# Optimization experiments

Hardware: AMD Instinct MI355X
Metric: run time of the kernel (lower is better)

The kernel has to match this reference:

```python
import jax, jax.numpy as jnp
import numpy as np

B, S, D, H, DFF = 4, 1024, 1024, 16, 4096
DK = D // H
EPS = 1e-6


def setup_inputs() -> dict:
    key = jax.random.key(0)
    ks = jax.random.split(key, 16)
    sd = 0.02
    inp = {
        "x_v": jax.random.normal(ks[0], (B, S, D), jnp.float32),
        "x_k": jax.random.normal(ks[1], (B, S, D), jnp.float32),
        "x_q": jax.random.normal(ks[2], (B, S, D), jnp.float32),
        "mask": jnp.zeros((B, 1, S), jnp.float32),
        # per-head projections stacked: [H, D, DK]
        "wq": jax.random.normal(ks[3], (H, D, DK), jnp.float32) * sd,
        "bq": jnp.zeros((H, DK), jnp.float32),
        "wk": jax.random.normal(ks[4], (H, D, DK), jnp.float32) * sd,
        "bk": jnp.zeros((H, DK), jnp.float32),
        "wv": jax.random.normal(ks[5], (H, D, DK), jnp.float32) * sd,
        "bv": jnp.zeros((H, DK), jnp.float32),
        "w0": jax.random.normal(ks[6], (D, D), jnp.float32) * sd,
        "b0": jnp.zeros((D,), jnp.float32),
        "ln1_g": jnp.ones((D,), jnp.float32),
        "ln1_b": jnp.zeros((D,), jnp.float32),
        "ff1_w": jax.random.normal(ks[7], (D, DFF), jnp.float32) * sd,
        "ff1_b": jnp.zeros((DFF,), jnp.float32),
        "ff2_w": jax.random.normal(ks[8], (DFF, D), jnp.float32) * sd,
        "ff2_b": jnp.zeros((D,), jnp.float32),
        "ln2_g": jnp.ones((D,), jnp.float32),
        "ln2_b": jnp.zeros((D,), jnp.float32),
    }
    return inp


def layer_norm(x, g, b):
    mu = jnp.mean(x, axis=-1, keepdims=True)
    var = jnp.mean(jnp.square(x - mu), axis=-1, keepdims=True)
    return (x - mu) * jax.lax.rsqrt(var + EPS) * g + b


def reference(x_v, x_k, x_q, mask, wq, bq, wk, bk, wv, bv, w0, b0,
              ln1_g, ln1_b, ff1_w, ff1_b, ff2_w, ff2_b, ln2_g, ln2_b):
    # --- Multi-head attention (heads batched instead of Python loop) ---
    q = jnp.einsum('bsd,hdk->bhsk', x_q, wq) + bq[:, None, :]  # [B,H,S,DK]
    k = jnp.einsum('bsd,hdk->bhsk', x_k, wk) + bk[:, None, :]
    v = jnp.einsum('bsd,hdk->bhsk', x_v, wv) + bv[:, None, :]
    scores = jnp.einsum('bhqk,bhsk->bhqs', q, k) / jnp.sqrt(jnp.float32(DK))
    scores = scores + mask[:, None, :, :] * (-1e9)  # mask broadcast over heads
    attn_w = jax.nn.softmax(scores, axis=-1)        # [B,H,S,S]
    attn = jnp.einsum('bhqs,bhsk->bhqk', attn_w, v)  # [B,H,S,DK]
    concat = attn.transpose(0, 2, 1, 3).reshape(B, S, D)
    mha_out = concat @ w0 + b0
    # --- Residual + LayerNorm 1 (dropout is identity at inference) ---
    sub1 = layer_norm(x_q + mha_out, ln1_g, ln1_b)
    # --- Point-wise FFN ---
    ffn = jax.nn.relu(sub1 @ ff1_w + ff1_b) @ ff2_w + ff2_b
    # --- Residual + LayerNorm 2 ---
    out = layer_norm(sub1 + ffn, ln2_g, ln2_b)
    # original returns the attention weights of the LAST head only
    return out, attn_w[:, -1]
```

## Files before the change

kernel.cpp:

```cpp
#include <hip/hip_runtime.h>
#include <hip/hip_bf16.h>
#include <stdint.h>

#define DEV __device__ __forceinline__

typedef uint16_t u16;
typedef __attribute__((ext_vector_type(8))) short s16x8;
typedef __attribute__((ext_vector_type(8))) unsigned short u16x8;
typedef __attribute__((ext_vector_type(4))) unsigned short u16x4;
typedef __attribute__((ext_vector_type(4))) float f32x4;

constexpr int CB = 4;
constexpr int CS = 1024;
constexpr int CD = 1024;
constexpr int CH = 16;
constexpr int CDFF = 4096;
constexpr int LSTR = 72;

DEV float b2f(u16 u) { union { uint32_t i; float f; } v; v.i = (uint32_t)u << 16; return v.f; }
DEV u16 f2b(float f) {
  union { float f; uint32_t i; } v; v.f = f;
  uint32_t r = v.i + 0x7fffu + ((v.i >> 16) & 1u);
  return (u16)(r >> 16);
}

using as1v = const __attribute__((address_space(1))) void;
using as3v = __attribute__((address_space(3))) void;
DEV void g2l16(const u16* g, u16* l) {
  __builtin_amdgcn_global_load_lds((as1v*)g, (as3v*)l, 16, 0, 0);
}

__global__ void detect_dtype(const uint32_t* __restrict__ w, uint32_t* __restrict__ flag) {
  if (threadIdx.x == 0 && blockIdx.x == 0) {
    flag[0] = (w[0] == 0x3F800000u) ? 1u : 0u;
    flag[1] = 0u;
  }
}

__global__ __launch_bounds__(256)
void cvt3(const void* __restrict__ s0, const void* __restrict__ s1, const void* __restrict__ s2,
          u16* __restrict__ d0, u16* __restrict__ d1, u16* __restrict__ d2,
          const uint32_t* __restrict__ flag)
{
  const void* s = blockIdx.z == 0 ? s0 : (blockIdx.z == 1 ? s1 : s2);
  u16* d        = blockIdx.z == 0 ? d0 : (blockIdx.z == 1 ? d1 : d2);
  size_t i = ((size_t)blockIdx.x * 256 + threadIdx.x) * 4;
  if (flag[0]) {
    const float* f = (const float*)s;
    u16x4 o;
#pragma unroll
    for (int j = 0; j < 4; j++) o[j] = f2b(f[i + j]);
    *(u16x4*)(d + i) = o;
  } else {
    *(u16x4*)(d + i) = *(const u16x4*)((const u16*)s + i);
  }
}

struct SmallCvt {
  const void* src[11];
  u16* dst[11];
  int n[11];
};
__global__ __launch_bounds__(256)
void cvt_small(SmallCvt sc, const uint32_t* __restrict__ flag)
{
  int idx = blockIdx.x * 256 + threadIdx.x;
#pragma unroll
  for (int a = 0; a < 11; a++) {
    if (idx < sc.n[a]) {
      if (flag[0]) sc.dst[a][idx] = f2b(((const float*)sc.src[a])[idx]);
      else         sc.dst[a][idx] = ((const u16*)sc.src[a])[idx];
      return;
    }
    idx -= sc.n[a];
  }
}

__global__ __launch_bounds__(256)
void transpose64d(const void* __restrict__ in, u16* __restrict__ out,
                  int in_rs, long long in_ys, long long in_zs,
                  int out_rs, long long out_ys, long long out_zs,
                  const uint32_t* __restrict__ flag)
{
  int t = blockIdx.x * 256 + threadIdx.x;
  int k  = t & 63;
  int n8 = t >> 6;
  size_t ib = (size_t)blockIdx.z * in_zs + (size_t)blockIdx.y * in_ys
            + (size_t)n8 * 8 * in_rs + k;
  u16* ob = out + (size_t)blockIdx.z * out_zs + (size_t)blockIdx.y * out_ys
                + (size_t)k * out_rs + (size_t)n8 * 8;
  u16x8 v;
  if (flag[0]) {
    const float* f = (const float*)in;
#pragma unroll
    for (int j = 0; j < 8; j++) v[j] = f2b(f[ib + (size_t)j * in_rs]);
  } else {
    const u16* u = (const u16*)in;
#pragma unroll
    for (int j = 0; j < 8; j++) v[j] = u[ib + (size_t)j * in_rs];
  }
  *(u16x8*)ob = v;
}

struct GemmArgs {
  const u16* A[3];
  const u16* Bt[3];
  const u16* bias[3];
  u16* C[3];
  float scales[3];
  int M, N, K;
  int relu;
};

template<int MI, int NI, int WGM, int WGN>
DEV void gemm_body(const GemmArgs& g)
{
  constexpr int BM = WGM * MI * 16;
  constexpr int BN = WGN * NI * 16;
  constexpr int CHA = BM / 32;
  constexpr int CHB = BN / 32;

  const int z = blockIdx.z;
  const u16* __restrict__ A    = g.A[z];
  const u16* __restrict__ Bt   = g.Bt[z];
  const u16* __restrict__ bias = g.bias[z];
  u16* __restrict__ C          = g.C[z];
  const float scale = g.scales[z];
  const int N = g.N, K = g.K;

  __shared__ __align__(16) u16 lA[BM * 64];
  __shared__ __align__(16) u16 lB[BN * 64];

  const int tid  = threadIdx.x;
  const int lane = tid & 63;
  const int wave = tid >> 6;
  const int quad = lane >> 4;
  const int l16  = lane & 15;
  const int sw   = l16 & 7;
  const int wm = (wave / WGN) * MI * 16;
  const int wn = (wave % WGN) * NI * 16;

  const int flat = blockIdx.y * gridDim.x + blockIdx.x;
  const int nY = gridDim.y;
  const size_t bm = (size_t)(flat % nY) * BM;
  const size_t bn = (size_t)(flat / nY) * BN;

  f32x4 acc[MI][NI];
#pragma unroll
  for (int mi = 0; mi < MI; mi++)
#pragma unroll
    for (int ni = 0; ni < NI; ni++)
#pragma unroll
      for (int r = 0; r < 4; r++) acc[mi][ni][r] = 0.f;

  const u16* Ab = A + bm * K;
  const u16* Bb = Bt + bn * K;

  for (int k0 = 0; k0 < K; k0 += 64) {
#pragma unroll
    for (int i = 0; i < CHA; i++) {
      int c = i * 256 + tid;
      int r = c >> 3, j = c & 7;
      g2l16(Ab + (size_t)r * K + k0 + ((j ^ (r & 7)) * 8), lA + c * 8);
    }
#pragma unroll
    for (int i = 0; i < CHB; i++) {
      int c = i * 256 + tid;
      int r = c >> 3, j = c & 7;
      g2l16(Bb + (size_t)r * K + k0 + ((j ^ (r & 7)) * 8), lB + c * 8);
    }
    __syncthreads();
#pragma unroll
    for (int kk = 0; kk < 2; kk++) {
      s16x8 af[MI], bfr[NI];
#pragma unroll
      for (int mi = 0; mi < MI; mi++)
        af[mi] = *(const s16x8*)(lA + (wm + mi * 16 + l16) * 64 + (((kk * 4 + quad) ^ sw) * 8));
#pragma unroll
      for (int ni = 0; ni < NI; ni++)
        bfr[ni] = *(const s16x8*)(lB + (wn + ni * 16 + l16) * 64 + (((kk * 4 + quad) ^ sw) * 8));
#pragma unroll
      for (int mi = 0; mi < MI; mi++)
#pragma unroll
        for (int ni = 0; ni < NI; ni++)
          acc[mi][ni] = __builtin_amdgcn_mfma_f32_16x16x32_bf16(af[mi], bfr[ni], acc[mi][ni], 0, 0, 0);
    }
    __syncthreads();
  }

  float bvals[NI];
#pragma unroll
  for (int ni = 0; ni < NI; ni++) bvals[ni] = b2f(bias[bn + wn + ni * 16 + l16]);
#pragma unroll
  for (int mi = 0; mi < MI; mi++) {
#pragma unroll
    for (int r = 0; r < 4; r++) {
      size_t row = bm + wm + mi * 16 + quad * 4 + r;
      u16* crow = C + row * N + bn + wn;
#pragma unroll
      for (int ni = 0; ni < NI; ni++) {
        float v = (acc[mi][ni][r] + bvals[ni]) * scale;
        if (g.relu) v = fmaxf(v, 0.f);
        crow[ni * 16 + l16] = f2b(v);
      }
    }
  }
}

__global__ __launch_bounds__(256, 4) void gemm_qkv (GemmArgs g) { gemm_body<4, 4, 2, 2>(g); }
__global__ __launch_bounds__(256, 4) void gemm_wo  (GemmArgs g) { gemm_body<2, 2, 2, 2>(g); }
__global__ __launch_bounds__(256, 4) void gemm_ffn1(GemmArgs g) { gemm_body<4, 4, 2, 2>(g); }
__global__ __launch_bounds__(256, 4) void gemm_ffn2(GemmArgs g) { gemm_body<2, 2, 2, 2>(g); }

__global__ __launch_bounds__(256, 4)
void flash_attn(const u16* __restrict__ Qb, const u16* __restrict__ Kb,
                const u16* __restrict__ Vt, const u16* __restrict__ mask,
                u16* __restrict__ O, float* __restrict__ ml)
{
  const int b = blockIdx.z;
  const int h = blockIdx.x & 15;
  const int q0 = (blockIdx.x >> 4) * 64;
  const int tid  = threadIdx.x;
  const int lane = tid & 63, wave = tid >> 6;
  const int quad = lane >> 4, l16 = lane & 15;

  __shared__ __align__(16) u16 lK[64 * LSTR];
  __shared__ __align__(16) u16 lV[64 * LSTR];
  __shared__ __align__(16) u16 lP[4][16 * LSTR];

  s16x8 aq[2];
  {
    const u16* qp = Qb + ((size_t)b * CS + q0 + wave * 16 + l16) * CD + h * 64 + quad * 8;
    aq[0] = *(const s16x8*)qp;
    aq[1] = *(const s16x8*)(qp + 32);
  }

  f32x4 of[4];
  float m_r[4], l_r[4];
#pragma unroll
  for (int nt = 0; nt < 4; nt++)
#pragma unroll
    for (int r = 0; r < 4; r++) of[nt][r] = 0.f;
#pragma unroll
  for (int r = 0; r < 4; r++) { m_r[r] = -3.0e38f; l_r[r] = 0.f; }

  int srow[2], scol[2];
#pragma unroll
  for (int i = 0; i < 2; i++) {
    int c = i * 256 + tid;
    srow[i] = c >> 3;
    scol[i] = (c & 7) * 8;
  }

  const u16* Kbase = Kb + (size_t)b * CS * CD + h * 64;
  const u16* Vbase = Vt + ((size_t)(b * CH + h)) * 64 * CS;
  u16* lPw = lP[wave];

  for (int kt = 0; kt < CS / 64; kt++) {
    u16x8 rk[2], rv[2];
#pragma unroll
    for (int i = 0; i < 2; i++) {
      rk[i] = *(const u16x8*)(Kbase + (size_t)(kt * 64 + srow[i]) * CD + scol[i]);
      rv[i] = *(const u16x8*)(Vbase + (size_t)srow[i] * CS + kt * 64 + scol[i]);
    }
    __syncthreads();
#pragma unroll
    for (int i = 0; i < 2; i++) {
      *(u16x8*)(lK + srow[i] * LSTR + scol[i]) = rk[i];
      *(u16x8*)(lV + srow[i] * LSTR + scol[i]) = rv[i];
    }
    __syncthreads();

    f32x4 sf[4];
#pragma unroll
    for (int ni = 0; ni < 4; ni++)
#pragma unroll
      for (int r = 0; r < 4; r++) sf[ni][r] = 0.f;
#pragma unroll
    for (int kk = 0; kk < 2; kk++) {
#pragma unroll
      for (int ni = 0; ni < 4; ni++) {
        s16x8 bk = *(const s16x8*)(lK + (ni * 16 + l16) * LSTR + kk * 32 + quad * 8);
        sf[ni] = __builtin_amdgcn_mfma_f32_16x16x32_bf16(aq[kk], bk, sf[ni], 0, 0, 0);
      }
    }
#pragma unroll
    for (int ni = 0; ni < 4; ni++) {
      float mv = b2f(mask[(size_t)b * CS + kt * 64 + ni * 16 + l16]) * -1e9f;
#pragma unroll
      for (int r = 0; r < 4; r++) sf[ni][r] += mv;
    }
    float mx[4];
#pragma unroll
    for (int r = 0; r < 4; r++)
      mx[r] = fmaxf(fmaxf(sf[0][r], sf[1][r]), fmaxf(sf[2][r], sf[3][r]));
#pragma unroll
    for (int off = 1; off < 16; off <<= 1)
#pragma unroll
      for (int r = 0; r < 4; r++) mx[r] = fmaxf(mx[r], __shfl_xor(mx[r], off, 16));
    float al[4], ps[4];
#pragma unroll
    for (int r = 0; r < 4; r++) {
      float mn = fmaxf(m_r[r], mx[r]);
      al[r] = __expf(m_r[r] - mn);
      m_r[r] = mn;
      ps[r] = 0.f;
    }
#pragma unroll
    for (int ni = 0; ni < 4; ni++)
#pragma unroll
      for (int r = 0; r < 4; r++) {
        float p = __expf(sf[ni][r] - m_r[r]);
        sf[ni][r] = p;
        ps[r] += p;
      }
#pragma unroll
    for (int off = 1; off < 16; off <<= 1)
#pragma unroll
      for (int r = 0; r < 4; r++) ps[r] += __shfl_xor(ps[r], off, 16);
#pragma unroll
    for (int r = 0; r < 4; r++) l_r[r] = l_r[r] * al[r] + ps[r];
#pragma unroll
    for (int nt = 0; nt < 4; nt++)
#pragma unroll
      for (int r = 0; r < 4; r++) of[nt][r] *= al[r];
#pragma unroll
    for (int ni = 0; ni < 4; ni++)
#pragma unroll
      for (int r = 0; r < 4; r++)
        lPw[(quad * 4 + r) * LSTR + ni * 16 + l16] = f2b(sf[ni][r]);
    __syncthreads();
#pragma unroll
    for (int kk = 0; kk < 2; kk++) {
      s16x8 ap = *(const s16x8*)(lPw + l16 * LSTR + kk * 32 + quad * 8);
#pragma unroll
      for (int nt = 0; nt < 4; nt++) {
        s16x8 bv = *(const s16x8*)(lV + (nt * 16 + l16) * LSTR + kk * 32 + quad * 8);
        of[nt] = __builtin_amdgcn_mfma_f32_16x16x32_bf16(ap, bv, of[nt], 0, 0, 0);
      }
    }
  }

#pragma unroll
  for (int r = 0; r < 4; r++) {
    float inv = 1.f / l_r[r];
    size_t row = q0 + wave * 16 + quad * 4 + r;
    u16* orow = O + ((size_t)b * CS + row) * CD + h * 64;
#pragma unroll
    for (int nt = 0; nt < 4; nt++) orow[nt * 16 + l16] = f2b(of[nt][r] * inv);
    if (h == CH - 1 && l16 == 0) {
      ml[(size_t)b * CS + row] = m_r[r];
      ml[(size_t)CB * CS + (size_t)b * CS + row] = l_r[r];
    }
  }
}

__global__ __launch_bounds__(256)
void attn_probs(const u16* __restrict__ Qb, const u16* __restrict__ Kb,
                const u16* __restrict__ mask, const float* __restrict__ ml,
                void* __restrict__ outbuf, const uint32_t* __restrict__ flag)
{
  const int b = blockIdx.z;
  const int h = CH - 1;
  const int q0 = blockIdx.x * 64;
  const int tid  = threadIdx.x;
  const int lane = tid & 63, wave = tid >> 6;
  const int quad = lane >> 4, l16 = lane & 15;
  const size_t OUT1 = (size_t)CB * CS * CD;
  const bool f32out = flag[0] != 0;

  __shared__ __align__(16) u16 lK[64 * LSTR];

  s16x8 aq[2];
  {
    const u16* qp = Qb + ((size_t)b * CS + q0 + wave * 16 + l16) * CD + h * 64 + quad * 8;
    aq[0] = *(const s16x8*)qp;
    aq[1] = *(const s16x8*)(qp + 32);
  }
  float mr[4], lr[4];
#pragma unroll
  for (int r = 0; r < 4; r++) {
    size_t row = q0 + wave * 16 + quad * 4 + r;
    mr[r] = ml[(size_t)b * CS + row];
    lr[r] = 1.f / ml[(size_t)CB * CS + (size_t)b * CS + row];
  }
  int srow[2], scol[2];
#pragma unroll
  for (int i = 0; i < 2; i++) {
    int c = i * 256 + tid;
    srow[i] = c >> 3;
    scol[i] = (c & 7) * 8;
  }
  const u16* Kbase = Kb + (size_t)b * CS * CD + h * 64;

  for (int kt = 0; kt < CS / 64; kt++) {
    u16x8 rk[2];
#pragma unroll
    for (int i = 0; i < 2; i++)
      rk[i] = *(const u16x8*)(Kbase + (size_t)(kt * 64 + srow[i]) * CD + scol[i]);
    __syncthreads();
#pragma unroll
    for (int i = 0; i < 2; i++)
      *(u16x8*)(lK + srow[i] * LSTR + scol[i]) = rk[i];
    __syncthreads();
    f32x4 sf[4];
#pragma unroll
    for (int ni = 0; ni < 4; ni++)
#pragma unroll
      for (int r = 0; r < 4; r++) sf[ni][r] = 0.f;
#pragma unroll
    for (int kk = 0; kk < 2; kk++) {
#pragma unroll
      for (int ni = 0; ni < 4; ni++) {
        s16x8 bk = *(const s16x8*)(lK + (ni * 16 + l16) * LSTR + kk * 32 + quad * 8);
        sf[ni] = __builtin_amdgcn_mfma_f32_16x16x32_bf16(aq[kk], bk, sf[ni], 0, 0, 0);
      }
    }
#pragma unroll
    for (int ni = 0; ni < 4; ni++) {
      float mv = b2f(mask[(size_t)b * CS + kt * 64 + ni * 16 + l16]) * -1e9f;
#pragma unroll
      for (int r = 0; r < 4; r++) {
        float p = __expf(sf[ni][r] + mv - mr[r]) * lr[r];
        size_t row = q0 + wave * 16 + quad * 4 + r;
        size_t idx = OUT1 + ((size_t)b * CS + row) * CS + kt * 64 + ni * 16 + l16;
        if (f32out) ((float*)outbuf)[idx] = p;
        else        ((u16*)outbuf)[idx] = f2b(p);
      }
    }
  }
}

__global__ __launch_bounds__(256)
void resid_ln(const u16* __restrict__ x, const u16* __restrict__ y,
              const u16* __restrict__ g, const u16* __restrict__ bb,
              void* __restrict__ out, const uint32_t* __restrict__ flag,
              int to_out)
{
  const int row = blockIdx.x;
  const int tid = threadIdx.x;
  __shared__ float rs[4], rs2[4];
  const u16* xr = x + (size_t)row * CD;
  const u16* yr = y + (size_t)row * CD;
  const int base = tid * 4;
  const bool f32out = to_out && (flag[0] != 0);
  float v[4];
  float s = 0.f, s2 = 0.f;
#pragma unroll
  for (int i = 0; i < 4; i++) {
    float a = b2f(xr[base + i]) + b2f(yr[base + i]);
    v[i] = a; s += a; s2 += a * a;
  }
#pragma unroll
  for (int off = 32; off > 0; off >>= 1) {
    s += __shfl_down(s, off, 64);
    s2 += __shfl_down(s2, off, 64);
  }
  if ((tid & 63) == 0) { rs[tid >> 6] = s; rs2[tid >> 6] = s2; }
  __syncthreads();
  float st = rs[0] + rs[1] + rs[2] + rs[3];
  float s2t = rs2[0] + rs2[1] + rs2[2] + rs2[3];
  float mu = st * (1.f / CD);
  float var = s2t * (1.f / CD) - mu * mu;
  float rstd = rsqrtf(var + 1e-6f);
#pragma unroll
  for (int i = 0; i < 4; i++) {
    float o = (v[i] - mu) * rstd * b2f(g[base + i]) + b2f(bb[base + i]);
    size_t idx = (size_t)row * CD + base + i;
    if (f32out) ((float*)out)[idx] = o;
    else        ((u16*)out)[idx] = f2b(o);
  }
}

extern "C" void kernel_launch(void* const* d_in, const int* in_sizes, int n_in,
                              void* d_out, int out_size, void* d_ws, size_t ws_size,
                              hipStream_t stream) {
  const void* x_v   = d_in[0];
  const void* x_k   = d_in[1];
  const void* x_q   = d_in[2];
  const void* maskI = d_in[3];
  const void* wq    = d_in[4];
  const void* bq    = d_in[5];
  const void* wk    = d_in[6];
  const void* bk    = d_in[7];
  const void* wv    = d_in[8];
  const void* bv    = d_in[9];
  const void* w0    = d_in[10];
  const void* b0    = d_in[11];
  const void* ln1_g = d_in[12];
  const void* ln1_b = d_in[13];
  const void* ff1_w = d_in[14];
  const void* ff1_b = d_in[15];
  const void* ff2_w = d_in[16];
  const void* ff2_b = d_in[17];
  const void* ln2_g = d_in[18];
  const void* ln2_b = d_in[19];

  u16* ws = (u16*)d_ws;
  size_t off = 0;
  auto alloc = [&](size_t n) { u16* p = ws + off; off += n; return p; };
  const size_t M1 = 1024 * 1024;
  u16* wqT   = alloc(M1);
  u16* wkT   = alloc(M1);
  u16* wvT   = alloc(M1);
  u16* w0T   = alloc(M1);
  u16* ff1T  = alloc(4 * M1);
  u16* ff2T  = alloc(4 * M1);
  u16* Qb    = alloc(4 * M1);
  u16* Kbuf  = alloc(4 * M1);
  u16* Vbuf  = alloc(4 * M1);
  u16* VtB   = alloc(4 * M1);
  u16* Ob    = alloc(4 * M1);
  u16* mha   = alloc(4 * M1);
  u16* sub1  = alloc(4 * M1);
  u16* ffmid = alloc(16 * M1);
  u16* cxq   = alloc(4 * M1);
  u16* cxk   = alloc(4 * M1);
  u16* cxv   = alloc(4 * M1);
  u16* cmask = alloc(4096);
  u16* cbq   = alloc(1024);
  u16* cbk   = alloc(1024);
  u16* cbv   = alloc(1024);
  u16* cb0   = alloc(1024);
  u16* cf1b  = alloc(4096);
  u16* cf2b  = alloc(1024);
  u16* cl1g  = alloc(1024);
  u16* cl1b  = alloc(1024);
  u16* cl2g  = alloc(1024);
  u16* cl2b  = alloc(1024);
  float* ml  = (float*)alloc(16384);
  uint32_t* flag = (uint32_t*)alloc(64);
  if (ws_size < off * sizeof(u16)) return;

  dim3 blk(256);

  detect_dtype<<<dim3(1), dim3(64), 0, stream>>>((const uint32_t*)ln1_g, flag);
  const uint32_t* fIn = flag;
  const uint32_t* fBf = flag + 1;

  cvt3<<<dim3(4096, 1, 3), blk, 0, stream>>>(x_q, x_k, x_v, cxq, cxk, cxv, fIn);
  {
    SmallCvt sc{};
    const void* s[11] = {maskI, bq, bk, bv, b0, ff1_b, ff2_b, ln1_g, ln1_b, ln2_g, ln2_b};
    u16* d[11] = {cmask, cbq, cbk, cbv, cb0, cf1b, cf2b, cl1g, cl1b, cl2g, cl2b};
    int n[11] = {4096, 1024, 1024, 1024, 1024, 4096, 1024, 1024, 1024, 1024, 1024};
    for (int i = 0; i < 11; i++) { sc.src[i] = s[i]; sc.dst[i] = d[i]; sc.n[i] = n[i]; }
    cvt_small<<<dim3(68), blk, 0, stream>>>(sc, fIn);
  }

  transpose64d<<<dim3(32, 16, 1), blk, 0, stream>>>(wq, wqT, 64, (long long)CD * 64, 0, CD, 64LL * CD, 0, fIn);
  transpose64d<<<dim3(32, 16, 1), blk, 0, stream>>>(wk, wkT, 64, (long long)CD * 64, 0, CD, 64LL * CD, 0, fIn);
  transpose64d<<<dim3(32, 16, 1), blk, 0, stream>>>(wv, wvT, 64, (long long)CD * 64, 0, CD, 64LL * CD, 0, fIn);
  transpose64d<<<dim3(32, 16, 1), blk, 0, stream>>>(w0, w0T, CD, 64, 0, CD, 64LL * CD, 0, fIn);
  transpose64d<<<dim3(32, 64, 1), blk, 0, stream>>>(ff1_w, ff1T, CDFF, 64, 0, CD, 64LL * CD, 0, fIn);
  transpose64d<<<dim3(128, 16, 1), blk, 0, stream>>>(ff2_w, ff2T, CD, 64, 0, CDFF, 64LL * CDFF, 0, fIn);

  {
    GemmArgs ga{};
    ga.A[0] = cxq;  ga.A[1] = cxk;  ga.A[2] = cxv;
    ga.Bt[0] = wqT; ga.Bt[1] = wkT; ga.Bt[2] = wvT;
    ga.bias[0] = cbq; ga.bias[1] = cbk; ga.bias[2] = cbv;
    ga.C[0] = Qb; ga.C[1] = Kbuf; ga.C[2] = Vbuf;
    ga.scales[0] = 0.125f; ga.scales[1] = 1.f; ga.scales[2] = 1.f;
    ga.M = CB * CS; ga.N = CD; ga.K = CD; ga.relu = 0;
    gemm_qkv<<<dim3(8, 32, 3), blk, 0, stream>>>(ga);
  }

  transpose64d<<<dim3(32, 16, 4), blk, 0, stream>>>(Vbuf, VtB, CD, 64, (long long)CS * CD,
                                                    CS, 64LL * CS, (long long)CH * 64 * CS, fBf);

  flash_attn<<<dim3(256, 1, CB), blk, 0, stream>>>(Qb, Kbuf, VtB, cmask, Ob, ml);

  attn_probs<<<dim3(CS / 64, 1, CB), blk, 0, stream>>>(Qb, Kbuf, cmask, ml, d_out, fIn);

  {
    GemmArgs ga{};
    ga.A[0] = Ob; ga.Bt[0] = w0T; ga.bias[0] = cb0; ga.C[0] = mha;
    ga.scales[0] = 1.f;
    ga.M = CB * CS; ga.N = CD; ga.K = CD; ga.relu = 0;
    gemm_wo<<<dim3(16, 64, 1), blk, 0, stream>>>(ga);
  }

  resid_ln<<<dim3(CB * CS), blk, 0, stream>>>(cxq, mha, cl1g, cl1b, sub1, fIn, 0);

  {
    GemmArgs ga{};
    ga.A[0] = sub1; ga.Bt[0] = ff1T; ga.bias[0] = cf1b; ga.C[0] = ffmid;
    ga.scales[0] = 1.f;
    ga.M = CB * CS; ga.N = CDFF; ga.K = CD; ga.relu = 1;
    gemm_ffn1<<<dim3(32, 32, 1), blk, 0, stream>>>(ga);
  }

  {
    GemmArgs ga{};
    ga.A[0] = ffmid; ga.Bt[0] = ff2T; ga.bias[0] = cf2b; ga.C[0] = mha;
    ga.scales[0] = 1.f;
    ga.M = CB * CS; ga.N = CD; ga.K = CDFF; ga.relu = 0;
    gemm_ffn2<<<dim3(16, 64, 1), blk, 0, stream>>>(ga);
  }

  resid_ln<<<dim3(CB * CS), blk, 0, stream>>>(sub1, mha, cl2g, cl2b, d_out, fIn, 1);
}
```

Measured before the change: 451.2 us.

## Prefetch next K/V tile into registers and XOR-swizzle LDS in attention kernels

Both attention kernels now issue global loads for the next K/V tile right after the current tile is stored to LDS, so global latency overlaps the MFMA and softmax work. LDS tiles drop the padded stride in favour of an XOR swizzle on 16-byte chunks, which shrinks shared memory and is meant to avoid bank conflicts. The barrier before the P·V stage is removed because each wave only reads its own P buffer. This adds register pressure from the held prefetch registers, and the swizzle math must match between the write and read sides.

```diff
diff --git a/kernel.cpp b/kernel.cpp
--- a/kernel.cpp
+++ b/kernel.cpp
@@ -223,9 +223,10 @@
   const int tid  = threadIdx.x;
   const int lane = tid & 63, wave = tid >> 6;
   const int quad = lane >> 4, l16 = lane & 15;
-
-  __shared__ __align__(16) u16 lK[64 * LSTR];
-  __shared__ __align__(16) u16 lV[64 * LSTR];
+  const int swz = l16 & 7;
+
+  __shared__ __align__(16) u16 lK[64 * 64];
+  __shared__ __align__(16) u16 lV[64 * 64];
   __shared__ __align__(16) u16 lP[4][16 * LSTR];
 
   s16x8 aq[2];
@@ -244,32 +245,42 @@
 #pragma unroll
   for (int r = 0; r < 4; r++) { m_r[r] = -3.0e38f; l_r[r] = 0.f; }
 
-  int srow[2], scol[2];
+  int srow[2], sj[2], wOff[2];
 #pragma unroll
   for (int i = 0; i < 2; i++) {
     int c = i * 256 + tid;
     srow[i] = c >> 3;
-    scol[i] = (c & 7) * 8;
+    sj[i]   = c & 7;
+    wOff[i] = srow[i] * 64 + ((sj[i] ^ (srow[i] & 7)) * 8);
   }
 
   const u16* Kbase = Kb + (size_t)b * CS * CD + h * 64;
   const u16* Vbase = Vt + ((size_t)(b * CH + h)) * 64 * CS;
   u16* lPw = lP[wave];
 
+  u16x8 rk[2], rv[2];
+#pragma unroll
+  for (int i = 0; i < 2; i++) {
+    rk[i] = *(const u16x8*)(Kbase + (size_t)srow[i] * CD + sj[i] * 8);
+    rv[i] = *(const u16x8*)(Vbase + (size_t)srow[i] * CS + sj[i] * 8);
+  }
+
   for (int kt = 0; kt < CS / 64; kt++) {
-    u16x8 rk[2], rv[2];
+    __syncthreads();
 #pragma unroll
     for (int i = 0; i < 2; i++) {
-      rk[i] = *(const u16x8*)(Kbase + (size_t)(kt * 64 + srow[i]) * CD + scol[i]);
-      rv[i] = *(const u16x8*)(Vbase + (size_t)srow[i] * CS + kt * 64 + scol[i]);
+      *(u16x8*)(lK + wOff[i]) = rk[i];
+      *(u16x8*)(lV + wOff[i]) = rv[i];
     }
     __syncthreads();
-#pragma unroll
-    for (int i = 0; i < 2; i++) {
-      *(u16x8*)(lK + srow[i] * LSTR + scol[i]) = rk[i];
-      *(u16x8*)(lV + srow[i] * LSTR + scol[i]) = rv[i];
-    }
-    __syncthreads();
+
+    if (kt + 1 < CS / 64) {
+#pragma unroll
+      for (int i = 0; i < 2; i++) {
+        rk[i] = *(const u16x8*)(Kbase + (size_t)((kt + 1) * 64 + srow[i]) * CD + sj[i] * 8);
+        rv[i] = *(const u16x8*)(Vbase + (size_t)srow[i] * CS + (kt + 1) * 64 + sj[i] * 8);
+      }
+    }
 
     f32x4 sf[4];
 #pragma unroll
@@ -280,7 +291,7 @@
     for (int kk = 0; kk < 2; kk++) {
 #pragma unroll
       for (int ni = 0; ni < 4; ni++) {
-        s16x8 bk = *(const s16x8*)(lK + (ni * 16 + l16) * LSTR + kk * 32 + quad * 8);
+        s16x8 bk = *(const s16x8*)(lK + (ni * 16 + l16) * 64 + (((kk * 4 + quad) ^ swz) * 8));
         sf[ni] = __builtin_amdgcn_mfma_f32_16x16x32_bf16(aq[kk], bk, sf[ni], 0, 0, 0);
       }
     }
@@ -329,13 +340,12 @@
 #pragma unroll
       for (int r = 0; r < 4; r++)
         lPw[(quad * 4 + r) * LSTR + ni * 16 + l16] = f2b(sf[ni][r]);
-    __syncthreads();
 #pragma unroll
     for (int kk = 0; kk < 2; kk++) {
       s16x8 ap = *(const s16x8*)(lPw + l16 * LSTR + kk * 32 + quad * 8);
 #pragma unroll
       for (int nt = 0; nt < 4; nt++) {
-        s16x8 bv = *(const s16x8*)(lV + (nt * 16 + l16) * LSTR + kk * 32 + quad * 8);
+        s16x8 bv = *(const s16x8*)(lV + (nt * 16 + l16) * 64 + (((kk * 4 + quad) ^ swz) * 8));
         of[nt] = __builtin_amdgcn_mfma_f32_16x16x32_bf16(ap, bv, of[nt], 0, 0, 0);
       }
     }
@@ -366,10 +376,11 @@
   const int tid  = threadIdx.x;
   const int lane = tid & 63, wave = tid >> 6;
   const int quad = lane >> 4, l16 = lane & 15;
+  const int swz = l16 & 7;
   const size_t OUT1 = (size_t)CB * CS * CD;
   const bool f32out = flag[0] != 0;
 
-  __shared__ __align__(16) u16 lK[64 * LSTR];
+  __shared__ __align__(16) u16 lK[64 * 64];
 
   s16x8 aq[2];
   {
@@ -384,25 +395,32 @@
     mr[r] = ml[(size_t)b * CS + row];
     lr[r] = 1.f / ml[(size_t)CB * CS + (size_t)b * CS + row];
   }
-  int srow[2], scol[2];
+  int srow[2], sj[2], wOff[2];
 #pragma unroll
   for (int i = 0; i < 2; i++) {
     int c = i * 256 + tid;
     srow[i] = c >> 3;
-    scol[i] = (c & 7) * 8;
+    sj[i]   = c & 7;
+    wOff[i] = srow[i] * 64 + ((sj[i] ^ (srow[i] & 7)) * 8);
   }
   const u16* Kbase = Kb + (size_t)b * CS * CD + h * 64;
 
+  u16x8 rk[2];
+#pragma unroll
+  for (int i = 0; i < 2; i++)
+    rk[i] = *(const u16x8*)(Kbase + (size_t)srow[i] * CD + sj[i] * 8);
+
   for (int kt = 0; kt < CS / 64; kt++) {
-    u16x8 rk[2];
+    __syncthreads();
 #pragma unroll
     for (int i = 0; i < 2; i++)
-      rk[i] = *(const u16x8*)(Kbase + (size_t)(kt * 64 + srow[i]) * CD + scol[i]);
+      *(u16x8*)(lK + wOff[i]) = rk[i];
     __syncthreads();
-#pragma unroll
-    for (int i = 0; i < 2; i++)
-      *(u16x8*)(lK + srow[i] * LSTR + scol[i]) = rk[i];
-    __syncthreads();
+    if (kt + 1 < CS / 64) {
+#pragma unroll
+      for (int i = 0; i < 2; i++)
+        rk[i] = *(const u16x8*)(Kbase + (size_t)((kt + 1) * 64 + srow[i]) * CD + sj[i] * 8);
+    }
     f32x4 sf[4];
 #pragma unroll
     for (int ni = 0; ni < 4; ni++)
@@ -412,7 +430,7 @@
     for (int kk = 0; kk < 2; kk++) {
 #pragma unroll
       for (int ni = 0; ni < 4; ni++) {
-        s16x8 bk = *(const s16x8*)(lK + (ni * 16 + l16) * LSTR + kk * 32 + quad * 8);
+        s16x8 bk = *(const s16x8*)(lK + (ni * 16 + l16) * 64 + (((kk * 4 + quad) ^ swz) * 8));
         sf[ni] = __builtin_amdgcn_mfma_f32_16x16x32_bf16(aq[kk], bk, sf[ni], 0, 0, 0);
       }
     }
```

Result: no change. 446.5 us (-1.0%).
